# Kernel optimization log

Measured on AMD Instinct MI355X. Metric: run time of the kernel, lower is better.

The kernel has to match this reference:

```python
import jax, jax.numpy as jnp
import numpy as np

N, T, n, C, C2 = 4, 8, 16384, 64, 64

def setup_inputs() -> dict:
    key = jax.random.key(0)
    k1, k2, k3, k4, k5 = jax.random.split(key, 5)
    return {
        "key_mem": jax.random.normal(k1, (N, T, n, C), dtype=jnp.float32),
        "val_mem": jax.random.normal(k2, (N, T, n, C2), dtype=jnp.float32),
        "key_cur": jax.random.normal(k3, (N, n, C), dtype=jnp.float32),
        "val_cur": jax.random.normal(k4, (N, n, C2), dtype=jnp.float32),
        "alpha": jax.random.normal(k5, (1,), dtype=jnp.float32),
    }

def reference(key_mem, val_mem, key_cur, val_cur, alpha):
    # kv_mul: contract memory tokens (T*n) -> (N, C, C2), tiny matrix
    kv_mul = jnp.einsum('btnc,btnd->bcd', key_mem, val_mem)
    # softmax over the C axis (dim=1 in torch layout (N, C, C2))
    kv_mul = jax.nn.softmax(kv_mul, axis=1)
    # out: (N, n, C) @ (N, C, C2) -> (N, n, C2)
    out = jnp.einsum('bnc,bcd->bnd', key_cur, kv_mul)
    return alpha * out + val_cur
```

## Files before the change

### kernel.cpp

```cpp
#include <hip/hip_runtime.h>
#include <math.h>

#define N_TOK   16384
#define K_TOT   (8 * N_TOK)
#define N_BATCH 4
#define BPB     128
#define RPB     (K_TOT / BPB)
#define CHUNK   64
#define NCH     (RPB / CHUNK)


typedef float f32x4 __attribute__((ext_vector_type(4)));

__device__ __forceinline__ void gload16(const float* g, float* l) {
  __builtin_amdgcn_global_load_lds(
      (const __attribute__((address_space(1))) void*)g,
      (__attribute__((address_space(3))) void*)l, 16, 0, 0);
}

#define WAIT_VM0   0x0F70u
#define WAIT_LGKM0 0xC07Fu

__global__ __launch_bounds__(512, 2) void k1_outer(
    const float* __restrict__ key, const float* __restrict__ val,
    float* __restrict__ part) {
  __shared__ float lds[2][8192];

  int blk  = blockIdx.x;
  int b    = blk / BPB;
  int p    = blk % BPB;
  int t    = threadIdx.x;
  int wave = t >> 6;
  int lane = t & 63;

  size_t base = ((size_t)b * K_TOT + (size_t)p * RPB) * 64;

  const float* sarr = (wave < 4) ? (key + base) : (val + base);
  uint ldsarr = (wave < 4) ? 0u : 4096u;
  uint uoff   = (uint)((wave & 3) * 1024);

  int half = t >> 8;
  int tid  = t & 255;
  int c4   = tid >> 4;
  int d4   = tid & 15;
  int r0   = half * 32;

  float acc[4][4];
#pragma unroll
  for (int i = 0; i < 4; i++)
#pragma unroll
    for (int j = 0; j < 4; j++) acc[i][j] = 0.f;

  auto stage = [&](int ch, int par) {
    const float* g = sarr + (size_t)ch * (CHUNK * 64) + uoff + lane * 4;
    float* l = &lds[par][ldsarr + uoff];
#pragma unroll
    for (int q = 0; q < 4; q++)
      gload16(g + q * 256, l + q * 256);
  };

  auto compute = [&](int par) {
    const float* Kb = &lds[par][(r0 << 6) + c4 * 4];
    const float* Vb = &lds[par][4096 + (r0 << 6) + d4 * 4];
#pragma unroll
    for (int r = 0; r < 32; r++) {
      float4 kk = *(const float4*)&Kb[r * 64];
      float4 vv = *(const float4*)&Vb[r * 64];
#pragma unroll
      for (int i = 0; i < 4; i++)
#pragma unroll
        for (int j = 0; j < 4; j++)
          acc[i][j] = fmaf((&kk.x)[i], (&vv.x)[j], acc[i][j]);
    }
  };

  stage(0, 0);
  asm volatile("" ::: "memory");
  __builtin_amdgcn_s_waitcnt(WAIT_VM0);
  __builtin_amdgcn_s_barrier();
  asm volatile("" ::: "memory");

#pragma unroll 2
  for (int ch = 0; ch < NCH; ch++) {
    if (ch + 1 < NCH) stage(ch + 1, (ch + 1) & 1);
    compute(ch & 1);
    asm volatile("" ::: "memory");
    __builtin_amdgcn_s_waitcnt(WAIT_VM0);
    __builtin_amdgcn_s_barrier();
    asm volatile("" ::: "memory");
  }

  float* scratch = &lds[0][0];
  if (half) {
#pragma unroll
    for (int i = 0; i < 4; i++)
      *(float4*)&scratch[tid * 20 + i * 4] =
          make_float4(acc[i][0], acc[i][1], acc[i][2], acc[i][3]);
  }
  asm volatile("" ::: "memory");
  __builtin_amdgcn_s_waitcnt(WAIT_LGKM0);
  __builtin_amdgcn_s_barrier();
  asm volatile("" ::: "memory");
  if (!half) {
    float* dst = part + (size_t)blk * 4096;
#pragma unroll
    for (int i = 0; i < 4; i++) {
      float4 s = *(const float4*)&scratch[tid * 20 + i * 4];
      float4 o = make_float4(acc[i][0] + s.x, acc[i][1] + s.y,
                             acc[i][2] + s.z, acc[i][3] + s.w);
      *(float4*)&dst[(c4 * 4 + i) * 64 + d4 * 4] = o;
    }
  }
}

__global__ __launch_bounds__(256, 4) void k2_reduce(
    const float* __restrict__ part, float* __restrict__ kv, int bpb) {
  int b  = blockIdx.x >> 6;
  int c  = blockIdx.x & 63;
  int p4 = threadIdx.x >> 6;
  int d  = threadIdx.x & 63;

  float s = 0.f;
  int iters = bpb >> 2;
  const float* src = part + (size_t)(b * bpb) * 4096 + c * 64 + d;
#pragma unroll 4
  for (int x = 0; x < iters; x++) s += src[(size_t)(p4 + 4 * x) * 4096];

  __shared__ float l[256];
  l[threadIdx.x] = s;
  __syncthreads();
  if (p4 == 0)
    kv[((size_t)b * 64 + c) * 64 + d] = l[d] + l[64 + d] + l[128 + d] + l[192 + d];
}

__global__ __launch_bounds__(256, 4) void k3_out(
    const float* __restrict__ kv, const float* __restrict__ keyc,
    const float* __restrict__ valc, const float* __restrict__ alphap,
    float* __restrict__ out) {
  __shared__ float Ps[4096];
  __shared__ float kT[64 * 68];
  __shared__ float redm[4][64];
  __shared__ float reds[4][64];

  int bb = blockIdx.x >> 8;
  int mb = blockIdx.x & 255;
  int m0 = mb * 64;
  int t = threadIdx.x;

  int d  = t & 63;
  int cg = t >> 6;
  const float* kvb = kv + (size_t)bb * 4096;
  float v[16];
  float mx = -3.0e38f;
#pragma unroll
  for (int i = 0; i < 16; i++) {
    v[i] = kvb[(cg * 16 + i) * 64 + d];
    mx = fmaxf(mx, v[i]);
  }
  redm[cg][d] = mx;

  int r  = t >> 2;
  int cb = (t & 3) * 16;
  const float* krow = keyc + ((size_t)bb * N_TOK + m0 + r) * 64;
#pragma unroll
  for (int u = 0; u < 4; u++) {
    float4 kk = *(const float4*)&krow[cb + 4 * u];
    int c = cb + 4 * u;
    kT[(c + 0) * 68 + r] = kk.x;
    kT[(c + 1) * 68 + r] = kk.y;
    kT[(c + 2) * 68 + r] = kk.z;
    kT[(c + 3) * 68 + r] = kk.w;
  }
  __syncthreads();

  mx = fmaxf(fmaxf(redm[0][d], redm[1][d]), fmaxf(redm[2][d], redm[3][d]));
  float s = 0.f;
#pragma unroll
  for (int i = 0; i < 16; i++) {
    float e = __expf(v[i] - mx);
    Ps[(cg * 16 + i) * 64 + d] = e;
    s += e;
  }
  reds[cg][d] = s;
  __syncthreads();

  int wave = t >> 6, lane = t & 63;
  int mi = lane >> 3, j = lane & 7;
  int m = wave * 16 + mi * 2;

  float acc[2][8];
#pragma unroll
  for (int a = 0; a < 2; a++)
#pragma unroll
    for (int dd = 0; dd < 8; dd++) acc[a][dd] = 0.f;

#pragma unroll 4
  for (int c = 0; c < 64; c++) {
    float2 kk = *(const float2*)&kT[c * 68 + m];
    float4 p0 = *(const float4*)&Ps[c * 64 + 8 * j];
    float4 p1 = *(const float4*)&Ps[c * 64 + 8 * j + 4];
    float pr[8] = {p0.x, p0.y, p0.z, p0.w, p1.x, p1.y, p1.z, p1.w};
#pragma unroll
    for (int dd = 0; dd < 8; dd++) {
      acc[0][dd] = fmaf(kk.x, pr[dd], acc[0][dd]);
      acc[1][dd] = fmaf(kk.y, pr[dd], acc[1][dd]);
    }
  }

  float alpha = alphap[0];
  float sc[8];
#pragma unroll
  for (int dd = 0; dd < 8; dd++) {
    int dq = 8 * j + dd;
    float den = reds[0][dq] + reds[1][dq] + reds[2][dq] + reds[3][dq];
    sc[dd] = alpha / den;
  }

#pragma unroll
  for (int a = 0; a < 2; a++) {
    size_t off = ((size_t)bb * N_TOK + m0 + m + a) * 64 + 8 * j;
    float4 v0 = *(const float4*)&valc[off];
    float4 v1 = *(const float4*)&valc[off + 4];
    float4 o0 = make_float4(fmaf(sc[0], acc[a][0], v0.x),
                            fmaf(sc[1], acc[a][1], v0.y),
                            fmaf(sc[2], acc[a][2], v0.z),
                            fmaf(sc[3], acc[a][3], v0.w));
    float4 o1 = make_float4(fmaf(sc[4], acc[a][4], v1.x),
                            fmaf(sc[5], acc[a][5], v1.y),
                            fmaf(sc[6], acc[a][6], v1.z),
                            fmaf(sc[7], acc[a][7], v1.w));
    *(float4*)&out[off] = o0;
    *(float4*)&out[off + 4] = o1;
  }
}

extern "C" void kernel_launch(void* const* d_in, const int* in_sizes, int n_in,
                              void* d_out, int out_size, void* d_ws,
                              size_t ws_size, hipStream_t stream) {
  const float* key_mem = (const float*)d_in[0];
  const float* val_mem = (const float*)d_in[1];
  const float* key_cur = (const float*)d_in[2];
  const float* val_cur = (const float*)d_in[3];
  const float* alpha   = (const float*)d_in[4];
  float* out = (float*)d_out;
  float* ws  = (float*)d_ws;

  float* part = ws;
  float* kv   = ws + (size_t)(N_BATCH * BPB) * 4096;

  k1_outer<<<N_BATCH * BPB, 512, 0, stream>>>(key_mem, val_mem, part);
  k2_reduce<<<256, 256, 0, stream>>>(part, kv, BPB);
  k3_out<<<N_BATCH * (N_TOK / 64), 256, 0, stream>>>(kv, key_cur, val_cur,
                                                     alpha, out);
}
```

Before: 357.6 us.

## Replace LDS-staged outer-product tiling with direct global loads per thread

Removes the double-buffered LDS staging (global_load_lds plus barriers) in the key-value outer-product kernel. Each thread now owns one key channel and eight value channels and reads both straight from global memory, relying on cache broadcast across lanes for the shared value rows. This drops barrier and LDS traffic, but each thread does only 8 FMAs per 9 loads instead of 16 FMAs per two float4 LDS reads, so reuse falls sharply and the kernel may become load-issue bound. Each lane also reads eight consecutive floats from the same row as all other lanes, which depends on the cache to avoid redundant fetches.

New measurement: 584.4 us. +63.4%, slower.

```diff
diff --git a/kernel.cpp b/kernel.cpp
--- a/kernel.cpp
+++ b/kernel.cpp
@@ -6,26 +6,10 @@
 #define N_BATCH 4
 #define BPB     128
 #define RPB     (K_TOT / BPB)
-#define CHUNK   64
-#define NCH     (RPB / CHUNK)
-
-
-typedef float f32x4 __attribute__((ext_vector_type(4)));
-
-__device__ __forceinline__ void gload16(const float* g, float* l) {
-  __builtin_amdgcn_global_load_lds(
-      (const __attribute__((address_space(1))) void*)g,
-      (__attribute__((address_space(3))) void*)l, 16, 0, 0);
-}
-
-#define WAIT_VM0   0x0F70u
-#define WAIT_LGKM0 0xC07Fu
 
 __global__ __launch_bounds__(512, 2) void k1_outer(
     const float* __restrict__ key, const float* __restrict__ val,
     float* __restrict__ part) {
-  __shared__ float lds[2][8192];
-
   int blk  = blockIdx.x;
   int b    = blk / BPB;
   int p    = blk % BPB;
@@ -34,83 +18,34 @@
   int lane = t & 63;
 
   size_t base = ((size_t)b * K_TOT + (size_t)p * RPB) * 64;
+  const float* Kp = key + base + lane;
+  const float* Vp = val + base + wave * 8;
 
-  const float* sarr = (wave < 4) ? (key + base) : (val + base);
-  uint ldsarr = (wave < 4) ? 0u : 4096u;
-  uint uoff   = (uint)((wave & 3) * 1024);
+  float acc[8];
+#pragma unroll
+  for (int j = 0; j < 8; j++) acc[j] = 0.f;
 
-  int half = t >> 8;
-  int tid  = t & 255;
-  int c4   = tid >> 4;
-  int d4   = tid & 15;
-  int r0   = half * 32;
-
-  float acc[4][4];
+  for (int tk = 0; tk < RPB; tk += 8) {
 #pragma unroll
-  for (int i = 0; i < 4; i++)
-#pragma unroll
-    for (int j = 0; j < 4; j++) acc[i][j] = 0.f;
-
-  auto stage = [&](int ch, int par) {
-    const float* g = sarr + (size_t)ch * (CHUNK * 64) + uoff + lane * 4;
-    float* l = &lds[par][ldsarr + uoff];
-#pragma unroll
-    for (int q = 0; q < 4; q++)
-      gload16(g + q * 256, l + q * 256);
-  };
-
-  auto compute = [&](int par) {
-    const float* Kb = &lds[par][(r0 << 6) + c4 * 4];
-    const float* Vb = &lds[par][4096 + (r0 << 6) + d4 * 4];
-#pragma unroll
-    for (int r = 0; r < 32; r++) {
-      float4 kk = *(const float4*)&Kb[r * 64];
-      float4 vv = *(const float4*)&Vb[r * 64];
-#pragma unroll
-      for (int i = 0; i < 4; i++)
-#pragma unroll
-        for (int j = 0; j < 4; j++)
-          acc[i][j] = fmaf((&kk.x)[i], (&vv.x)[j], acc[i][j]);
+    for (int u = 0; u < 8; u++) {
+      size_t o = (size_t)(tk + u) * 64;
+      float  kk = Kp[o];
+      float4 v0 = *(const float4*)&Vp[o];
+      float4 v1 = *(const float4*)&Vp[o + 4];
+      acc[0] = fmaf(kk, v0.x, acc[0]);
+      acc[1] = fmaf(kk, v0.y, acc[1]);
+      acc[2] = fmaf(kk, v0.z, acc[2]);
+      acc[3] = fmaf(kk, v0.w, acc[3]);
+      acc[4] = fmaf(kk, v1.x, acc[4]);
+      acc[5] = fmaf(kk, v1.y, acc[5]);
+      acc[6] = fmaf(kk, v1.z, acc[6]);
+      acc[7] = fmaf(kk, v1.w, acc[7]);
     }
-  };
-
-  stage(0, 0);
-  asm volatile("" ::: "memory");
-  __builtin_amdgcn_s_waitcnt(WAIT_VM0);
-  __builtin_amdgcn_s_barrier();
-  asm volatile("" ::: "memory");
-
-#pragma unroll 2
-  for (int ch = 0; ch < NCH; ch++) {
-    if (ch + 1 < NCH) stage(ch + 1, (ch + 1) & 1);
-    compute(ch & 1);
-    asm volatile("" ::: "memory");
-    __builtin_amdgcn_s_waitcnt(WAIT_VM0);
-    __builtin_amdgcn_s_barrier();
-    asm volatile("" ::: "memory");
   }
 
-  float* scratch = &lds[0][0];
-  if (half) {
-#pragma unroll
-    for (int i = 0; i < 4; i++)
-      *(float4*)&scratch[tid * 20 + i * 4] =
-          make_float4(acc[i][0], acc[i][1], acc[i][2], acc[i][3]);
-  }
-  asm volatile("" ::: "memory");
-  __builtin_amdgcn_s_waitcnt(WAIT_LGKM0);
-  __builtin_amdgcn_s_barrier();
-  asm volatile("" ::: "memory");
-  if (!half) {
-    float* dst = part + (size_t)blk * 4096;
-#pragma unroll
-    for (int i = 0; i < 4; i++) {
-      float4 s = *(const float4*)&scratch[tid * 20 + i * 4];
-      float4 o = make_float4(acc[i][0] + s.x, acc[i][1] + s.y,
-                             acc[i][2] + s.z, acc[i][3] + s.w);
-      *(float4*)&dst[(c4 * 4 + i) * 64 + d4 * 4] = o;
-    }
-  }
+  float* dst = part + (size_t)blk * 4096 + lane * 64 + wave * 8;
+  *(float4*)dst       = make_float4(acc[0], acc[1], acc[2], acc[3]);
+  *(float4*)(dst + 4) = make_float4(acc[4], acc[5], acc[6], acc[7]);
 }
 
 __global__ __launch_bounds__(256, 4) void k2_reduce(
```
